# Kernel optimization log

Hardware: AMD Instinct MI355X
Metric: run time of the kernel (lower is better)

## Reference

```python
import jax, jax.numpy as jnp
import numpy as np

N_ATOMS = 100000
N_PAIRS = 2000000
N_EMB = 30
N_DIST = 100
N_HID = 60


def setup_inputs() -> dict:
    key = jax.random.key(0)
    ks = jax.random.split(key, 9)
    atom_features = jax.random.normal(ks[0], (N_ATOMS, N_EMB), dtype=jnp.float32)
    distance = jax.random.uniform(ks[1], (N_PAIRS, N_DIST), dtype=jnp.float32)
    # tf.segment_sum requires sorted segment ids
    distance_membership_i = jnp.sort(jax.random.randint(ks[2], (N_PAIRS,), 0, N_ATOMS))
    distance_membership_j = jax.random.randint(ks[3], (N_PAIRS,), 0, N_ATOMS)
    # glorot-uniform weights; biases small random (trainable, nonzero for a nontrivial reference)
    def glorot(k, fan_in, fan_out):
        lim = np.sqrt(6.0 / (fan_in + fan_out)).astype(np.float32)
        return jax.random.uniform(k, (fan_in, fan_out), minval=-lim, maxval=lim, dtype=jnp.float32)
    W_cf = glorot(ks[4], N_EMB, N_HID)
    W_df = glorot(ks[5], N_DIST, N_HID)
    W_fc = glorot(ks[6], N_HID, N_EMB)
    b_cf = 0.1 * jax.random.normal(ks[7], (N_HID,), dtype=jnp.float32)
    b_df = 0.1 * jax.random.normal(ks[8], (N_HID,), dtype=jnp.float32)
    return dict(atom_features=atom_features, distance=distance,
                distance_membership_i=distance_membership_i,
                distance_membership_j=distance_membership_j,
                W_cf=W_cf, W_df=W_df, W_fc=W_fc, b_cf=b_cf, b_df=b_df)


def reference(atom_features, distance, distance_membership_i, distance_membership_j,
              W_cf, W_df, W_fc, b_cf, b_df):
    n_atoms = atom_features.shape[0]
    # [E, H] and [N, H]
    distance_hidden = distance @ W_df + b_df
    atom_hidden = atom_features @ W_cf + b_cf
    # gather-fuse-matmul-activate over edges
    outputs = distance_hidden * atom_hidden[distance_membership_j]  # [E, H]
    outputs = jnp.tanh(outputs @ W_fc)                              # [E, F]
    # self-interaction correction term
    output_ii = jnp.tanh((b_df * atom_hidden) @ W_fc)               # [N, F]
    # scatter-reduce over destination atoms
    agg = jax.ops.segment_sum(outputs, distance_membership_i, num_segments=n_atoms)
    return agg - output_ii + atom_features
```

## Files before the change

kernel.cpp:

```cpp
#include <hip/hip_runtime.h>
#include <hip/hip_bf16.h>

#define N_ATOMS 100000
#define N_PAIRS 2000000
#define N_EMB 30
#define N_DIST 100
#define N_HID 60

#define TE 64
#define NTILES (N_PAIRS / TE)
#define EBLOCKS 768

typedef short bf16x8 __attribute__((ext_vector_type(8)));
typedef float f32x4 __attribute__((ext_vector_type(4)));

__device__ __forceinline__ ushort f2bf(float f) {
    __hip_bfloat16 h = __float2bfloat16(f);
    return __builtin_bit_cast(ushort, h);
}
__device__ __forceinline__ float bf2f(ushort u) {
    __hip_bfloat16 h = __builtin_bit_cast(__hip_bfloat16, u);
    return __bfloat162float(h);
}
__device__ __forceinline__ float fast_tanh(float x) {
    float e = __expf(2.0f * x);
    return 1.0f - 2.0f / (e + 1.0f);
}

__global__ __launch_bounds__(256) void atom_kernel(
    const float* __restrict__ af, const float* __restrict__ W_cf,
    const float* __restrict__ W_fc, const float* __restrict__ b_cf,
    const float* __restrict__ b_df, float* __restrict__ ah_out,
    float* __restrict__ out)
{
    __shared__ __align__(16) float ah_lds[4][N_HID];
    const int wave = threadIdx.x >> 6;
    const int lane = threadIdx.x & 63;
    const int n = blockIdx.x * 4 + wave;

    float ahv = 0.f;
    if (lane < N_HID) {
        ahv = b_cf[lane];
        #pragma unroll
        for (int k = 0; k < N_EMB; ++k)
            ahv = fmaf(af[(size_t)n * N_EMB + k], W_cf[k * N_HID + lane], ahv);
        ah_out[(size_t)n * N_HID + lane] = ahv;
        ah_lds[wave][lane] = ahv * b_df[lane];
    }
    __syncthreads();
    if (lane < N_EMB) {
        float s = 0.f;
        #pragma unroll
        for (int h = 0; h < N_HID; ++h)
            s = fmaf(ah_lds[wave][h], W_fc[h * N_EMB + lane], s);
        out[(size_t)n * N_EMB + lane] =
            af[(size_t)n * N_EMB + lane] - fast_tanh(s);
    }
}

__global__ __launch_bounds__(256, 3) void edge_kernel(
    const float* __restrict__ dist,
    const int* __restrict__ mi, const int* __restrict__ mj,
    const float* __restrict__ W_df, const float* __restrict__ W_fc,
    const float* __restrict__ b_df, const float* __restrict__ ah,
    float* out)
{
    __shared__ ushort A_lds[2][TE * 136];
    __shared__ ushort T_lds[TE * 72];
    __shared__ ushort S_lds[32 * 72];
    __shared__ int    mis[2][TE], mjs[2][TE];
    __shared__ int    seg_lds[TE];
    __shared__ int    seg_atom[TE];

    const int tid = threadIdx.x;
    const int wv = tid >> 6, lane = tid & 63;
    const int l4 = lane >> 4, ln = lane & 15;
    const int h1 = wv * 16 + ln;

    bf16x8 wdf_hi[4], wdf_lo[4];
    #pragma unroll
    for (int ks = 0; ks < 4; ++ks) {
        #pragma unroll
        for (int i = 0; i < 8; ++i) {
            int k = ks * 32 + l4 * 8 + i;
            float f = (k < N_DIST && h1 < N_HID) ? W_df[k * N_HID + h1] : 0.f;
            ushort hi = f2bf(f);
            wdf_hi[ks][i] = (short)hi;
            wdf_lo[ks][i] = (short)f2bf(f - bf2f(hi));
        }
    }
    bf16x8 wfc[2][2];
    #pragma unroll
    for (int nf = 0; nf < 2; ++nf) {
        #pragma unroll
        for (int ks = 0; ks < 2; ++ks) {
            #pragma unroll
            for (int i = 0; i < 8; ++i) {
                int k = ks * 32 + l4 * 8 + i;
                int n = nf * 16 + ln;
                float f = (k < N_HID && n < N_EMB) ? W_fc[k * N_EMB + n] : 0.f;
                wfc[nf][ks][i] = (short)f2bf(f);
            }
        }
    }
    const float bdf1 = (h1 < N_HID) ? b_df[h1] : 0.f;

    for (int idx = tid; idx < 2 * TE * 36; idx += 256) {
        int b = idx / (TE * 36), rem = idx % (TE * 36);
        int r = rem / 36, c = 100 + rem % 36;
        A_lds[b][r * 136 + c] = 0;
    }

    const int t0 = (int)(((long long)blockIdx.x * NTILES) / EBLOCKS);
    const int t1 = (int)(((long long)(blockIdx.x + 1) * NTILES) / EBLOCKS);

    f32x4 pf[7];
    int pmi = 0, pmj = 0;

    auto stage_issue = [&](int t) {
        const f32x4* src = (const f32x4*)(dist + (size_t)t * TE * N_DIST);
        #pragma unroll
        for (int k = 0; k < 6; ++k)
            pf[k] = __builtin_nontemporal_load(&src[k * 256 + tid]);
        if (tid < 64) {
            pf[6] = __builtin_nontemporal_load(&src[6 * 256 + tid]);
            pmi = mi[t * TE + tid];
            pmj = mj[t * TE + tid];
        }
    };
    auto stage_write = [&](int buf) {
        #pragma unroll
        for (int k = 0; k < 7; ++k) {
            int idx = k * 256 + tid;
            if (k < 6 || tid < 64) {
                int r = idx / 25, c = idx % 25;
                f32x4 v = pf[k];
                ushort4 pk2;
                pk2.x = f2bf(v[0]); pk2.y = f2bf(v[1]);
                pk2.z = f2bf(v[2]); pk2.w = f2bf(v[3]);
                *(ushort4*)&A_lds[buf][r * 136 + c * 4] = pk2;
            }
        }
        if (tid < 64) { mis[buf][tid] = pmi; mjs[buf][tid] = pmj; }
    };

    stage_issue(t0);
    stage_write(0);
    __syncthreads();

    int cur = 0;
    for (int t = t0; t < t1; ++t) {
        const bool hasnext = (t + 1 < t1);

        float ahg[4][4];
        #pragma unroll
        for (int m = 0; m < 4; ++m) {
            #pragma unroll
            for (int r = 0; r < 4; ++r) {
                int el = 16 * m + l4 * 4 + r;
                int j = mjs[cur][el];
                ahg[m][r] = (h1 < N_HID) ? ah[(size_t)j * N_HID + h1] : 0.f;
            }
        }

        if (hasnext) stage_issue(t + 1);

        f32x4 acc1[4] = {{0,0,0,0},{0,0,0,0},{0,0,0,0},{0,0,0,0}};
        #pragma unroll
        for (int ks = 0; ks < 4; ++ks) {
            #pragma unroll
            for (int m = 0; m < 4; ++m) {
                bf16x8 a = *(const bf16x8*)&A_lds[cur][(16 * m + ln) * 136 + ks * 32 + l4 * 8];
                acc1[m] = __builtin_amdgcn_mfma_f32_16x16x32_bf16(a, wdf_hi[ks], acc1[m], 0, 0, 0);
                acc1[m] = __builtin_amdgcn_mfma_f32_16x16x32_bf16(a, wdf_lo[ks], acc1[m], 0, 0, 0);
            }
        }


        #pragma unroll
        for (int m = 0; m < 4; ++m) {
            #pragma unroll
            for (int r = 0; r < 4; ++r) {
                int row = 16 * m + l4 * 4 + r;
                float tv = (acc1[m][r] + bdf1) * ahg[m][r];
                T_lds[row * 72 + h1] = (h1 < N_HID) ? f2bf(tv) : (ushort)0;
            }
        }
        __syncthreads();

        f32x4 acc2[2] = {{0,0,0,0},{0,0,0,0}};
        #pragma unroll
        for (int ks = 0; ks < 2; ++ks) {
            bf16x8 a2 = *(const bf16x8*)&T_lds[(16 * wv + ln) * 72 + ks * 32 + l4 * 8];
            #pragma unroll
            for (int nf = 0; nf < 2; ++nf)
                acc2[nf] = __builtin_amdgcn_mfma_f32_16x16x32_bf16(a2, wfc[nf][ks], acc2[nf], 0, 0, 0);
        }
        #pragma unroll
        for (int nf = 0; nf < 2; ++nf) {
            #pragma unroll
            for (int r = 0; r < 4; ++r) {
                int f = nf * 16 + ln;
                int e = 16 * wv + l4 * 4 + r;
                S_lds[f * 72 + e] = f2bf(fast_tanh(acc2[nf][r]));
            }
        }

        if (hasnext) stage_write(cur ^ 1);

        __syncthreads();

        int m_e = mis[cur][lane];
        int prevv = __shfl_up(m_e, 1);
        bool changed = (lane > 0) && (m_e != prevv);
        unsigned long long bmask = __ballot(changed);
        int segl = __popcll(bmask & ((2ull << lane) - 1ull));
        if (lane == 0 || changed) seg_atom[segl] = m_e;
        seg_lds[lane] = segl;
        int nseg = __popcll(bmask) + 1;

        int myseg = 16 * wv + ln;
        bf16x8 sfr[2];
        #pragma unroll
        for (int ks = 0; ks < 2; ++ks) {
            const int* sp = &seg_lds[ks * 32 + l4 * 8];
            #pragma unroll
            for (int i = 0; i < 8; ++i)
                sfr[ks][i] = (sp[i] == myseg) ? (short)0x3F80 : (short)0;
        }
        f32x4 acc3[2] = {{0,0,0,0},{0,0,0,0}};
        #pragma unroll
        for (int ks = 0; ks < 2; ++ks) {
            #pragma unroll
            for (int nf = 0; nf < 2; ++nf) {
                bf16x8 b = *(const bf16x8*)&S_lds[(nf * 16 + ln) * 72 + ks * 32 + l4 * 8];
                acc3[nf] = __builtin_amdgcn_mfma_f32_16x16x32_bf16(sfr[ks], b, acc3[nf], 0, 0, 0);
            }
        }
        #pragma unroll
        for (int nf = 0; nf < 2; ++nf) {
            #pragma unroll
            for (int r = 0; r < 4; ++r) {
                int gs = 16 * wv + l4 * 4 + r;
                int f = nf * 16 + ln;
                if (gs < nseg && f < N_EMB) {
                    int atomId = seg_atom[gs];
                    atomicAdd(&out[(size_t)atomId * N_EMB + f], acc3[nf][r]);
                }
            }
        }
        cur ^= 1;
    }
}

extern "C" void kernel_launch(void* const* d_in, const int* in_sizes, int n_in,
                              void* d_out, int out_size, void* d_ws, size_t ws_size,
                              hipStream_t stream) {
    const float* af   = (const float*)d_in[0];
    const float* dist = (const float*)d_in[1];
    const int*   mi   = (const int*)d_in[2];
    const int*   mj   = (const int*)d_in[3];
    const float* W_cf = (const float*)d_in[4];
    const float* W_df = (const float*)d_in[5];
    const float* W_fc = (const float*)d_in[6];
    const float* b_cf = (const float*)d_in[7];
    const float* b_df = (const float*)d_in[8];
    float* out = (float*)d_out;
    float* ah  = (float*)d_ws;

    atom_kernel<<<N_ATOMS / 4, 256, 0, stream>>>(af, W_cf, W_fc, b_cf, b_df, ah, out);
    edge_kernel<<<EBLOCKS, 256, 0, stream>>>(dist, mi, mj, W_df, W_fc, b_df, ah, out);
}
```

Measured before the change: 300.0 us.

## Drop split-bf16 weight correction and replace MFMA segment-sum with register run-length atomics

The distance-projection matmul now uses a single bf16 copy of W_df instead of a hi+lo split, halving the first-stage MFMA count at some precision cost. The segmented reduction, which used a one-hot MFMA over an LDS-staged tile, is replaced by per-lane run-length accumulation over 4 consecutive edges followed by atomicAdd. This removes the S_lds staging, the ballot and segment bookkeeping, and the third MFMA stage. In exchange it issues more global atomics, since runs are merged only within groups of 4 edges rather than across the 64-edge tile.

```diff
diff --git a/kernel.cpp b/kernel.cpp
--- a/kernel.cpp
+++ b/kernel.cpp
@@ -17,10 +17,6 @@
 __device__ __forceinline__ ushort f2bf(float f) {
     __hip_bfloat16 h = __float2bfloat16(f);
     return __builtin_bit_cast(ushort, h);
-}
-__device__ __forceinline__ float bf2f(ushort u) {
-    __hip_bfloat16 h = __builtin_bit_cast(__hip_bfloat16, u);
-    return __bfloat162float(h);
 }
 __device__ __forceinline__ float fast_tanh(float x) {
     float e = __expf(2.0f * x);
@@ -67,26 +63,21 @@
 {
     __shared__ ushort A_lds[2][TE * 136];
     __shared__ ushort T_lds[TE * 72];
-    __shared__ ushort S_lds[32 * 72];
     __shared__ int    mis[2][TE], mjs[2][TE];
-    __shared__ int    seg_lds[TE];
-    __shared__ int    seg_atom[TE];
 
     const int tid = threadIdx.x;
     const int wv = tid >> 6, lane = tid & 63;
     const int l4 = lane >> 4, ln = lane & 15;
     const int h1 = wv * 16 + ln;
 
-    bf16x8 wdf_hi[4], wdf_lo[4];
+    bf16x8 wdf[4];
     #pragma unroll
     for (int ks = 0; ks < 4; ++ks) {
         #pragma unroll
         for (int i = 0; i < 8; ++i) {
             int k = ks * 32 + l4 * 8 + i;
             float f = (k < N_DIST && h1 < N_HID) ? W_df[k * N_HID + h1] : 0.f;
-            ushort hi = f2bf(f);
-            wdf_hi[ks][i] = (short)hi;
-            wdf_lo[ks][i] = (short)f2bf(f - bf2f(hi));
+            wdf[ks][i] = (short)f2bf(f);
         }
     }
     bf16x8 wfc[2][2];
@@ -171,11 +162,9 @@
             #pragma unroll
             for (int m = 0; m < 4; ++m) {
                 bf16x8 a = *(const bf16x8*)&A_lds[cur][(16 * m + ln) * 136 + ks * 32 + l4 * 8];
-                acc1[m] = __builtin_amdgcn_mfma_f32_16x16x32_bf16(a, wdf_hi[ks], acc1[m], 0, 0, 0);
-                acc1[m] = __builtin_amdgcn_mfma_f32_16x16x32_bf16(a, wdf_lo[ks], acc1[m], 0, 0, 0);
-            }
-        }
-
+                acc1[m] = __builtin_amdgcn_mfma_f32_16x16x32_bf16(a, wdf[ks], acc1[m], 0, 0, 0);
+            }
+        }
 
         #pragma unroll
         for (int m = 0; m < 4; ++m) {
@@ -196,59 +185,38 @@
             for (int nf = 0; nf < 2; ++nf)
                 acc2[nf] = __builtin_amdgcn_mfma_f32_16x16x32_bf16(a2, wfc[nf][ks], acc2[nf], 0, 0, 0);
         }
-        #pragma unroll
-        for (int nf = 0; nf < 2; ++nf) {
-            #pragma unroll
-            for (int r = 0; r < 4; ++r) {
-                int f = nf * 16 + ln;
-                int e = 16 * wv + l4 * 4 + r;
-                S_lds[f * 72 + e] = f2bf(fast_tanh(acc2[nf][r]));
-            }
+
+        float s0v[4], s1v[4];
+        #pragma unroll
+        for (int r = 0; r < 4; ++r) {
+            s0v[r] = fast_tanh(acc2[0][r]);
+            s1v[r] = fast_tanh(acc2[1][r]);
+        }
+        {
+            int miv = mis[cur][16 * wv + ln];
+            int m_r[4];
+            #pragma unroll
+            for (int r = 0; r < 4; ++r) m_r[r] = __shfl(miv, l4 * 4 + r);
+
+            int cura = m_r[0];
+            float f0 = s0v[0], f1 = s1v[0];
+            #pragma unroll
+            for (int r = 1; r < 4; ++r) {
+                if (m_r[r] != cura) {
+                    atomicAdd(&out[(size_t)cura * N_EMB + ln], f0);
+                    if (ln < N_EMB - 16) atomicAdd(&out[(size_t)cura * N_EMB + 16 + ln], f1);
+                    cura = m_r[r]; f0 = s0v[r]; f1 = s1v[r];
+                } else {
+                    f0 += s0v[r]; f1 += s1v[r];
+                }
+            }
+            atomicAdd(&out[(size_t)cura * N_EMB + ln], f0);
+            if (ln < N_EMB - 16) atomicAdd(&out[(size_t)cura * N_EMB + 16 + ln], f1);
         }
 
         if (hasnext) stage_write(cur ^ 1);
 
         __syncthreads();
-
-        int m_e = mis[cur][lane];
-        int prevv = __shfl_up(m_e, 1);
-        bool changed = (lane > 0) && (m_e != prevv);
-        unsigned long long bmask = __ballot(changed);
-        int segl = __popcll(bmask & ((2ull << lane) - 1ull));
-        if (lane == 0 || changed) seg_atom[segl] = m_e;
-        seg_lds[lane] = segl;
-        int nseg = __popcll(bmask) + 1;
-
-        int myseg = 16 * wv + ln;
-        bf16x8 sfr[2];
-        #pragma unroll
-        for (int ks = 0; ks < 2; ++ks) {
-            const int* sp = &seg_lds[ks * 32 + l4 * 8];
-            #pragma unroll
-            for (int i = 0; i < 8; ++i)
-                sfr[ks][i] = (sp[i] == myseg) ? (short)0x3F80 : (short)0;
-        }
-        f32x4 acc3[2] = {{0,0,0,0},{0,0,0,0}};
-        #pragma unroll
-        for (int ks = 0; ks < 2; ++ks) {
-            #pragma unroll
-            for (int nf = 0; nf < 2; ++nf) {
-                bf16x8 b = *(const bf16x8*)&S_lds[(nf * 16 + ln) * 72 + ks * 32 + l4 * 8];
-                acc3[nf] = __builtin_amdgcn_mfma_f32_16x16x32_bf16(sfr[ks], b, acc3[nf], 0, 0, 0);
-            }
-        }
-        #pragma unroll
-        for (int nf = 0; nf < 2; ++nf) {
-            #pragma unroll
-            for (int r = 0; r < 4; ++r) {
-                int gs = 16 * wv + l4 * 4 + r;
-                int f = nf * 16 + ln;
-                if (gs < nseg && f < N_EMB) {
-                    int atomId = seg_atom[gs];
-                    atomicAdd(&out[(size_t)atomId * N_EMB + f], acc3[nf][r]);
-                }
-            }
-        }
         cur ^= 1;
     }
 }
```

Measured after the change: 451.7 us. 50.6% more time.

## Drop split-bf16 weights, prefetch next tile's atom gather, use LDS-only barriers

Applied to the files above, without the earlier changes.

Removes the hi/lo bf16 split of W_df, which halves the first-stage MFMAs but lowers the precision of the distance projection. The gather of atom_hidden rows for the next tile now runs right after the second barrier, so its global latency overlaps the segment-reduction and atomic phase. __syncthreads is replaced by a barrier that waits only on LDS counters, so in-flight global loads no longer stall it. The MFMA loop for the segment sum is also restructured slightly.

```diff
diff --git a/kernel.cpp b/kernel.cpp
--- a/kernel.cpp
+++ b/kernel.cpp
@@ -18,13 +18,15 @@
     __hip_bfloat16 h = __float2bfloat16(f);
     return __builtin_bit_cast(ushort, h);
 }
-__device__ __forceinline__ float bf2f(ushort u) {
-    __hip_bfloat16 h = __builtin_bit_cast(__hip_bfloat16, u);
-    return __bfloat162float(h);
-}
 __device__ __forceinline__ float fast_tanh(float x) {
     float e = __expf(2.0f * x);
     return 1.0f - 2.0f / (e + 1.0f);
+}
+
+__device__ __forceinline__ void lds_barrier() {
+    asm volatile("s_waitcnt lgkmcnt(0)" ::: "memory");
+    __builtin_amdgcn_s_barrier();
+    __builtin_amdgcn_sched_barrier(0);
 }
 
 __global__ __launch_bounds__(256) void atom_kernel(
@@ -77,16 +79,14 @@
     const int l4 = lane >> 4, ln = lane & 15;
     const int h1 = wv * 16 + ln;
 
-    bf16x8 wdf_hi[4], wdf_lo[4];
+    bf16x8 wdf[4];
     #pragma unroll
     for (int ks = 0; ks < 4; ++ks) {
         #pragma unroll
         for (int i = 0; i < 8; ++i) {
             int k = ks * 32 + l4 * 8 + i;
             float f = (k < N_DIST && h1 < N_HID) ? W_df[k * N_HID + h1] : 0.f;
-            ushort hi = f2bf(f);
-            wdf_hi[ks][i] = (short)hi;
-            wdf_lo[ks][i] = (short)f2bf(f - bf2f(hi));
+            wdf[ks][i] = (short)f2bf(f);
         }
     }
     bf16x8 wfc[2][2];
@@ -144,25 +144,28 @@
         if (tid < 64) { mis[buf][tid] = pmi; mjs[buf][tid] = pmj; }
     };
 
+    float ahg[4][4];
+    auto gather = [&](int buf) {
+        #pragma unroll
+        for (int m = 0; m < 4; ++m) {
+            #pragma unroll
+            for (int r = 0; r < 4; ++r) {
+                int el = 16 * m + l4 * 4 + r;
+                int j = mjs[buf][el];
+                ahg[m][r] = (h1 < N_HID) ? ah[(size_t)j * N_HID + h1] : 0.f;
+            }
+        }
+    };
+
     stage_issue(t0);
     stage_write(0);
     __syncthreads();
+    gather(0);
 
     int cur = 0;
     for (int t = t0; t < t1; ++t) {
         const bool hasnext = (t + 1 < t1);
 
-        float ahg[4][4];
-        #pragma unroll
-        for (int m = 0; m < 4; ++m) {
-            #pragma unroll
-            for (int r = 0; r < 4; ++r) {
-                int el = 16 * m + l4 * 4 + r;
-                int j = mjs[cur][el];
-                ahg[m][r] = (h1 < N_HID) ? ah[(size_t)j * N_HID + h1] : 0.f;
-            }
-        }
-
         if (hasnext) stage_issue(t + 1);
 
         f32x4 acc1[4] = {{0,0,0,0},{0,0,0,0},{0,0,0,0},{0,0,0,0}};
@@ -171,11 +174,9 @@
             #pragma unroll
             for (int m = 0; m < 4; ++m) {
                 bf16x8 a = *(const bf16x8*)&A_lds[cur][(16 * m + ln) * 136 + ks * 32 + l4 * 8];
-                acc1[m] = __builtin_amdgcn_mfma_f32_16x16x32_bf16(a, wdf_hi[ks], acc1[m], 0, 0, 0);
-                acc1[m] = __builtin_amdgcn_mfma_f32_16x16x32_bf16(a, wdf_lo[ks], acc1[m], 0, 0, 0);
-            }
-        }
-
+                acc1[m] = __builtin_amdgcn_mfma_f32_16x16x32_bf16(a, wdf[ks], acc1[m], 0, 0, 0);
+            }
+        }
 
         #pragma unroll
         for (int m = 0; m < 4; ++m) {
@@ -186,7 +187,7 @@
                 T_lds[row * 72 + h1] = (h1 < N_HID) ? f2bf(tv) : (ushort)0;
             }
         }
-        __syncthreads();
+        lds_barrier();
 
         f32x4 acc2[2] = {{0,0,0,0},{0,0,0,0}};
         #pragma unroll
@@ -208,7 +209,9 @@
 
         if (hasnext) stage_write(cur ^ 1);
 
-        __syncthreads();
+        lds_barrier();
+
+        if (hasnext) gather(cur ^ 1);
 
         int m_e = mis[cur][lane];
         int prevv = __shfl_up(m_e, 1);
@@ -220,21 +223,18 @@
         int nseg = __popcll(bmask) + 1;
 
         int myseg = 16 * wv + ln;
-        bf16x8 sfr[2];
+        f32x4 acc3[2] = {{0,0,0,0},{0,0,0,0}};
         #pragma unroll
         for (int ks = 0; ks < 2; ++ks) {
+            bf16x8 sfr;
             const int* sp = &seg_lds[ks * 32 + l4 * 8];
             #pragma unroll
             for (int i = 0; i < 8; ++i)
-                sfr[ks][i] = (sp[i] == myseg) ? (short)0x3F80 : (short)0;
-        }
-        f32x4 acc3[2] = {{0,0,0,0},{0,0,0,0}};
-        #pragma unroll
-        for (int ks = 0; ks < 2; ++ks) {
+                sfr[i] = (sp[i] == myseg) ? (short)0x3F80 : (short)0;
             #pragma unroll
             for (int nf = 0; nf < 2; ++nf) {
                 bf16x8 b = *(const bf16x8*)&S_lds[(nf * 16 + ln) * 72 + ks * 32 + l4 * 8];
-                acc3[nf] = __builtin_amdgcn_mfma_f32_16x16x32_bf16(sfr[ks], b, acc3[nf], 0, 0, 0);
+                acc3[nf] = __builtin_amdgcn_mfma_f32_16x16x32_bf16(sfr, b, acc3[nf], 0, 0, 0);
             }
         }
         #pragma unroll
```

After: 306.0 us. 2.0% more time.

## Drop split-bf16 weight correction and use packed hardware bf16 conversions

Applied to the files above, without the earlier changes.

Removes the hi/lo split of W_df so the distance projection uses one bf16 MFMA per tile instead of two, halving the first-GEMM matrix work. Replaces the software float-to-bf16 conversions with the packed v_cvt_pk_bf16_f32 instruction, precomputes the LDS staging offsets instead of dividing per write, and packs the tanh outputs into vectorized LDS stores. This trades accuracy in the distance projection for fewer instructions. The kernel is likely bound by streaming the distance array, so the gain may be small.

```diff
diff --git a/kernel.cpp b/kernel.cpp
--- a/kernel.cpp
+++ b/kernel.cpp
@@ -21,6 +21,14 @@
 __device__ __forceinline__ float bf2f(ushort u) {
     __hip_bfloat16 h = __builtin_bit_cast(__hip_bfloat16, u);
     return __bfloat162float(h);
+}
+__device__ __forceinline__ unsigned cvt_pk_bf16(float lo, float hi) {
+    unsigned r;
+    asm("v_cvt_pk_bf16_f32 %0, %1, %2" : "=v"(r) : "v"(lo), "v"(hi));
+    return r;
+}
+__device__ __forceinline__ ushort f2bf_rne(float x) {
+    return (ushort)cvt_pk_bf16(x, x);
 }
 __device__ __forceinline__ float fast_tanh(float x) {
     float e = __expf(2.0f * x);
@@ -77,16 +85,14 @@
     const int l4 = lane >> 4, ln = lane & 15;
     const int h1 = wv * 16 + ln;
 
-    bf16x8 wdf_hi[4], wdf_lo[4];
+    bf16x8 wdf[4];
     #pragma unroll
     for (int ks = 0; ks < 4; ++ks) {
         #pragma unroll
         for (int i = 0; i < 8; ++i) {
             int k = ks * 32 + l4 * 8 + i;
             float f = (k < N_DIST && h1 < N_HID) ? W_df[k * N_HID + h1] : 0.f;
-            ushort hi = f2bf(f);
-            wdf_hi[ks][i] = (short)hi;
-            wdf_lo[ks][i] = (short)f2bf(f - bf2f(hi));
+            wdf[ks][i] = (short)f2bf(f);
         }
     }
     bf16x8 wfc[2][2];
@@ -104,6 +110,13 @@
         }
     }
     const float bdf1 = (h1 < N_HID) ? b_df[h1] : 0.f;
+
+    int sdst[7];
+    #pragma unroll
+    for (int k = 0; k < 7; ++k) {
+        int idx = k * 256 + tid;
+        sdst[k] = (idx / 25) * 136 + (idx % 25) * 4;
+    }
 
     for (int idx = tid; idx < 2 * TE * 36; idx += 256) {
         int b = idx / (TE * 36), rem = idx % (TE * 36);
@@ -131,14 +144,12 @@
     auto stage_write = [&](int buf) {
         #pragma unroll
         for (int k = 0; k < 7; ++k) {
-            int idx = k * 256 + tid;
             if (k < 6 || tid < 64) {
-                int r = idx / 25, c = idx % 25;
                 f32x4 v = pf[k];
-                ushort4 pk2;
-                pk2.x = f2bf(v[0]); pk2.y = f2bf(v[1]);
-                pk2.z = f2bf(v[2]); pk2.w = f2bf(v[3]);
-                *(ushort4*)&A_lds[buf][r * 136 + c * 4] = pk2;
+                uint2 w;
+                w.x = cvt_pk_bf16(v[0], v[1]);
+                w.y = cvt_pk_bf16(v[2], v[3]);
+                *(uint2*)&A_lds[buf][sdst[k]] = w;
             }
         }
         if (tid < 64) { mis[buf][tid] = pmi; mjs[buf][tid] = pmj; }
@@ -171,11 +182,9 @@
             #pragma unroll
             for (int m = 0; m < 4; ++m) {
                 bf16x8 a = *(const bf16x8*)&A_lds[cur][(16 * m + ln) * 136 + ks * 32 + l4 * 8];
-                acc1[m] = __builtin_amdgcn_mfma_f32_16x16x32_bf16(a, wdf_hi[ks], acc1[m], 0, 0, 0);
-                acc1[m] = __builtin_amdgcn_mfma_f32_16x16x32_bf16(a, wdf_lo[ks], acc1[m], 0, 0, 0);
-            }
-        }
-
+                acc1[m] = __builtin_amdgcn_mfma_f32_16x16x32_bf16(a, wdf[ks], acc1[m], 0, 0, 0);
+            }
+        }
 
         #pragma unroll
         for (int m = 0; m < 4; ++m) {
@@ -183,7 +192,7 @@
             for (int r = 0; r < 4; ++r) {
                 int row = 16 * m + l4 * 4 + r;
                 float tv = (acc1[m][r] + bdf1) * ahg[m][r];
-                T_lds[row * 72 + h1] = (h1 < N_HID) ? f2bf(tv) : (ushort)0;
+                T_lds[row * 72 + h1] = f2bf_rne(tv);
             }
         }
         __syncthreads();
@@ -198,12 +207,10 @@
         }
         #pragma unroll
         for (int nf = 0; nf < 2; ++nf) {
-            #pragma unroll
-            for (int r = 0; r < 4; ++r) {
-                int f = nf * 16 + ln;
-                int e = 16 * wv + l4 * 4 + r;
-                S_lds[f * 72 + e] = f2bf(fast_tanh(acc2[nf][r]));
-            }
+            uint2 w;
+            w.x = cvt_pk_bf16(fast_tanh(acc2[nf][0]), fast_tanh(acc2[nf][1]));
+            w.y = cvt_pk_bf16(fast_tanh(acc2[nf][2]), fast_tanh(acc2[nf][3]));
+            *(uint2*)&S_lds[(nf * 16 + ln) * 72 + 16 * wv + l4 * 4] = w;
         }
 
         if (hasnext) stage_write(cur ^ 1);
@@ -220,21 +227,18 @@
         int nseg = __popcll(bmask) + 1;
 
         int myseg = 16 * wv + ln;
-        bf16x8 sfr[2];
+        f32x4 acc3[2] = {{0,0,0,0},{0,0,0,0}};
         #pragma unroll
         for (int ks = 0; ks < 2; ++ks) {
+            bf16x8 sfr;
             const int* sp = &seg_lds[ks * 32 + l4 * 8];
             #pragma unroll
             for (int i = 0; i < 8; ++i)
-                sfr[ks][i] = (sp[i] == myseg) ? (short)0x3F80 : (short)0;
-        }
-        f32x4 acc3[2] = {{0,0,0,0},{0,0,0,0}};
-        #pragma unroll
-        for (int ks = 0; ks < 2; ++ks) {
+                sfr[i] = (sp[i] == myseg) ? (short)0x3F80 : (short)0;
             #pragma unroll
             for (int nf = 0; nf < 2; ++nf) {
                 bf16x8 b = *(const bf16x8*)&S_lds[(nf * 16 + ln) * 72 + ks * 32 + l4 * 8];
-                acc3[nf] = __builtin_amdgcn_mfma_f32_16x16x32_bf16(sfr[ks], b, acc3[nf], 0, 0, 0);
+                acc3[nf] = __builtin_amdgcn_mfma_f32_16x16x32_bf16(sfr, b, acc3[nf], 0, 0, 0);
             }
         }
         #pragma unroll
```

After: 303.1 us. Within noise of the previous version (+1.0%).
